# Kernel optimization log

Measured on AMD Instinct MI355X. Metric: run time of the kernel, lower is better.

## Reference

```python
import jax, jax.numpy as jnp
import numpy as np

B, N, D, H = 4, 2048, 512, 8
HEAD = D // H
TEMP = 8.0


def setup_inputs() -> dict:
    key = jax.random.key(0)
    k1, k2, k3, k4 = jax.random.split(key, 4)
    return {
        "keys": jax.random.normal(k1, (B, N, D), dtype=jnp.float32),
        "queries": jax.random.normal(k2, (B, N, D), dtype=jnp.float32),
        "values": jax.random.normal(k3, (B, N, D), dtype=jnp.float32),
        "W_comb": jax.random.normal(k4, (D, D), dtype=jnp.float32) * (1.0 / np.sqrt(D)),
        "b_comb": jnp.zeros((D,), dtype=jnp.float32),
    }


def reference(keys, queries, values, W_comb, b_comb):
    b, nk, d = keys.shape
    nq = queries.shape[1]
    h, hd = H, HEAD
    # split heads: (b, n, d) -> (b, n, h, hd)
    k = keys.reshape(b, nk, h, hd)
    q = queries.reshape(b, nq, h, hd)
    v = values.reshape(b, nk, h, hd)
    # scaled dot-product attention per head
    logits = jnp.einsum("bqhd,bkhd->bhqk", q, k) / TEMP  # (b, h, nq, nk)
    w = jax.nn.softmax(logits, axis=-1)
    out = jnp.einsum("bhqk,bkhd->bqhd", w, v).reshape(b, nq, d)
    # head_combine: Linear with bias (torch: x @ W.T + b)
    return out @ W_comb.T + b_comb
```

## Files before the change

### kernel.cpp

```cpp
#include <hip/hip_runtime.h>

#define B_ 4
#define N_ 2048
#define D_ 512
#define H_ 8

typedef __attribute__((ext_vector_type(8))) short bf16x8;
typedef __attribute__((ext_vector_type(4))) short bf16x4;
typedef __attribute__((ext_vector_type(4))) float f32x4;

__device__ __forceinline__ unsigned short f32_to_bf16(float f) {
  unsigned int u = __float_as_uint(f);
  u += 0x7FFFu + ((u >> 16) & 1u);
  return (unsigned short)(u >> 16);
}

__device__ __forceinline__ unsigned int pack2_bf16(float a, float b) {
#if __has_builtin(__builtin_amdgcn_cvt_pk_bf16_f32)
  typedef __attribute__((ext_vector_type(2))) __bf16 bf16v2;
  bf16v2 r = __builtin_amdgcn_cvt_pk_bf16_f32(a, b);
  return *(unsigned int*)&r;
#else
  return (unsigned int)f32_to_bf16(a) | ((unsigned int)f32_to_bf16(b) << 16);
#endif
}

__device__ __forceinline__ float fast_exp2(float x) {
#if __has_builtin(__builtin_amdgcn_exp2f)
  return __builtin_amdgcn_exp2f(x);
#else
  return exp2f(x);
#endif
}

__device__ __forceinline__ f32x4 mfma16(bf16x4 a, bf16x4 b, f32x4 c) {
#if __has_builtin(__builtin_amdgcn_mfma_f32_16x16x16_bf16)
  return __builtin_amdgcn_mfma_f32_16x16x16_bf16(a, b, c, 0, 0, 0);
#else
  return __builtin_amdgcn_mfma_f32_16x16x16bf16_1k(a, b, c, 0, 0, 0);
#endif
}

__global__ __launch_bounds__(256) void convert_kernel(
    const float* __restrict__ Kf, const float* __restrict__ Qf,
    const float* __restrict__ Vf, const float* __restrict__ Wf,
    unsigned short* __restrict__ Qb, unsigned short* __restrict__ Kb,
    unsigned short* __restrict__ Wb, unsigned short* __restrict__ Vt) {
  __shared__ float tile[64 * 72];
  const int tid = threadIdx.x;
  if (blockIdx.x < 1024) {
    const float qs = 0.125f * 1.4426950408889634f;
    int gid = blockIdx.x * 256 + tid;
    const float4* Q4 = (const float4*)Qf;
    const float4* K4 = (const float4*)Kf;
    for (int i = gid; i < (B_ * N_ * D_) / 4; i += 262144) {
      float4 q = Q4[i];
      ((uint2*)Qb)[i] = make_uint2(pack2_bf16(q.x * qs, q.y * qs),
                                   pack2_bf16(q.z * qs, q.w * qs));
      float4 k = K4[i];
      ((uint2*)Kb)[i] = make_uint2(pack2_bf16(k.x, k.y), pack2_bf16(k.z, k.w));
    }
    if (gid < (D_ * D_) / 4) {
      float4 w = ((const float4*)Wf)[gid];
      ((uint2*)Wb)[gid] = make_uint2(pack2_bf16(w.x, w.y), pack2_bf16(w.z, w.w));
    }
  } else {
    int bid = blockIdx.x - 1024;
    int nt = bid & 31, bh = bid >> 5;
    int b = bh >> 3, h = bh & 7;
    int n0 = nt * 64;
#pragma unroll
    for (int i = 0; i < 4; ++i) {
      int idx = i * 256 + tid;
      int r = idx >> 4, c = idx & 15;
      *(float4*)&tile[r * 72 + c * 4] =
          *(const float4*)(Vf + (size_t)(b * N_ + n0 + r) * D_ + h * 64 + c * 4);
    }
    __syncthreads();
    int d = tid >> 2, c = tid & 3;
    unsigned int o[8];
#pragma unroll
    for (int j = 0; j < 8; ++j)
      o[j] = pack2_bf16(tile[(c * 16 + 2 * j) * 72 + d],
                        tile[(c * 16 + 2 * j + 1) * 72 + d]);
    unsigned short* dst = Vt + ((size_t)bh * 64 + d) * N_ + n0 + c * 16;
    *(bf16x8*)dst = *(bf16x8*)&o[0];
    *(bf16x8*)(dst + 8) = *(bf16x8*)&o[4];
  }
}

__global__ __launch_bounds__(256, 2) void attn_kernel(
    const unsigned short* __restrict__ Qb, const unsigned short* __restrict__ Kb,
    const unsigned short* __restrict__ Vt, unsigned short* __restrict__ Ob) {
  __shared__ unsigned short Kl[2][64 * 72];
  __shared__ unsigned short Vl[2][64 * 72];

  const int tid = threadIdx.x;
  const int w = tid >> 6;
  const int lane = tid & 63;
  const int lr = lane & 15;
  const int lq = lane >> 4;

  const int bh = blockIdx.y;
  const int qb = blockIdx.x * 128;
  const size_t slab = (size_t)(bh >> 3) * N_ * D_ + (size_t)(bh & 7) * 64;
  const unsigned short* kbase = Kb + slab;
  const unsigned short* vtbase = Vt + (size_t)bh * 64 * N_;

  bf16x8 qa[2][2];
#pragma unroll
  for (int g = 0; g < 2; ++g) {
    const unsigned short* qrow =
        Qb + slab + (size_t)(qb + w * 32 + g * 16 + lr) * D_;
    qa[g][0] = *(const bf16x8*)(qrow + 8 * lq);
    qa[g][1] = *(const bf16x8*)(qrow + 32 + 8 * lq);
  }

  f32x4 O[4][2];
#pragma unroll
  for (int i = 0; i < 4; ++i)
#pragma unroll
    for (int g = 0; g < 2; ++g) O[i][g] = (f32x4){0.f, 0.f, 0.f, 0.f};
  float l_g[2] = {0.f, 0.f};

  const int st_r = tid >> 3;
  const int st_c = tid & 7;

  {
    const unsigned short* ksrc = kbase + (size_t)st_r * D_ + st_c * 8;
    bf16x8 a = *(const bf16x8*)ksrc;
    bf16x8 b = *(const bf16x8*)(ksrc + (size_t)32 * D_);
    const unsigned short* vsrc = vtbase + (size_t)st_r * N_ + st_c * 8;
    bf16x8 c = *(const bf16x8*)vsrc;
    bf16x8 d = *(const bf16x8*)(vsrc + (size_t)32 * N_);
    *(bf16x8*)&Kl[0][st_r * 72 + st_c * 8] = a;
    *(bf16x8*)&Kl[0][(st_r + 32) * 72 + st_c * 8] = b;
    *(bf16x8*)&Vl[0][st_r * 72 + st_c * 8] = c;
    *(bf16x8*)&Vl[0][(st_r + 32) * 72 + st_c * 8] = d;
  }

  for (int kt = 0; kt < 32; ++kt) {
    const int p = kt & 1;
    __syncthreads();

    bf16x8 nk0, nk1, nv0, nv1;
    const bool more = (kt + 1) < 32;
    if (more) {
      const int kb1 = (kt + 1) * 64;
      const unsigned short* ksrc = kbase + (size_t)(kb1 + st_r) * D_ + st_c * 8;
      nk0 = *(const bf16x8*)ksrc;
      nk1 = *(const bf16x8*)(ksrc + (size_t)32 * D_);
      const unsigned short* vsrc = vtbase + (size_t)st_r * N_ + kb1 + st_c * 8;
      nv0 = *(const bf16x8*)vsrc;
      nv1 = *(const bf16x8*)(vsrc + (size_t)32 * N_);
    }

    f32x4 S[4][2];
#pragma unroll
    for (int nt = 0; nt < 4; ++nt) {
      bf16x8 kf0 = *(const bf16x8*)&Kl[p][(nt * 16 + lr) * 72 + 8 * lq];
      bf16x8 kf1 = *(const bf16x8*)&Kl[p][(nt * 16 + lr) * 72 + 32 + 8 * lq];
#pragma unroll
      for (int g = 0; g < 2; ++g) {
        S[nt][g] = __builtin_amdgcn_mfma_f32_16x16x32_bf16(
            kf0, qa[g][0], (f32x4){0.f, 0.f, 0.f, 0.f}, 0, 0, 0);
        S[nt][g] = __builtin_amdgcn_mfma_f32_16x16x32_bf16(kf1, qa[g][1],
                                                           S[nt][g], 0, 0, 0);
      }
    }

    bf16x4 pf[4][2];
#pragma unroll
    for (int nt = 0; nt < 4; ++nt)
#pragma unroll
      for (int g = 0; g < 2; ++g) {
        float p0 = fast_exp2(S[nt][g][0]);
        float p1 = fast_exp2(S[nt][g][1]);
        float p2 = fast_exp2(S[nt][g][2]);
        float p3 = fast_exp2(S[nt][g][3]);
        l_g[g] += (p0 + p1) + (p2 + p3);
        uint2 packed = make_uint2(pack2_bf16(p0, p1), pack2_bf16(p2, p3));
        pf[nt][g] = *(bf16x4*)&packed;
      }

#pragma unroll
    for (int dt = 0; dt < 4; ++dt) {
#pragma unroll
      for (int nt = 0; nt < 4; ++nt) {
        bf16x4 vf =
            *(const bf16x4*)&Vl[p][(dt * 16 + lr) * 72 + nt * 16 + 4 * lq];
#pragma unroll
        for (int g = 0; g < 2; ++g)
          O[dt][g] = mfma16(vf, pf[nt][g], O[dt][g]);
      }
    }

    if (more) {
      *(bf16x8*)&Kl[1 - p][st_r * 72 + st_c * 8] = nk0;
      *(bf16x8*)&Kl[1 - p][(st_r + 32) * 72 + st_c * 8] = nk1;
      *(bf16x8*)&Vl[1 - p][st_r * 72 + st_c * 8] = nv0;
      *(bf16x8*)&Vl[1 - p][(st_r + 32) * 72 + st_c * 8] = nv1;
    }
  }

#pragma unroll
  for (int g = 0; g < 2; ++g) {
    l_g[g] += __shfl_xor(l_g[g], 16);
    l_g[g] += __shfl_xor(l_g[g], 32);
  }

  __syncthreads();
  unsigned short* SR = &Kl[0][0];
#pragma unroll
  for (int g = 0; g < 2; ++g) {
    float linv = 1.0f / l_g[g];
#pragma unroll
    for (int dt = 0; dt < 4; ++dt) {
      float v0 = O[dt][g][0] * linv;
      float v1 = O[dt][g][1] * linv;
      float v2 = O[dt][g][2] * linv;
      float v3 = O[dt][g][3] * linv;
      uint2 packed = make_uint2(pack2_bf16(v0, v1), pack2_bf16(v2, v3));
      *(bf16x4*)&SR[(w * 32 + g * 16 + lr) * 72 + dt * 16 + lq * 4] =
          *(bf16x4*)&packed;
    }
  }
  __syncthreads();
  {
    const int row = tid >> 1, half = tid & 1;
    unsigned short* dst = Ob + slab + (size_t)(qb + row) * D_ + half * 32;
    const unsigned short* src = &SR[row * 72 + half * 32];
    *(bf16x8*)dst = *(const bf16x8*)src;
    *(bf16x8*)(dst + 8) = *(const bf16x8*)(src + 8);
    *(bf16x8*)(dst + 16) = *(const bf16x8*)(src + 16);
    *(bf16x8*)(dst + 24) = *(const bf16x8*)(src + 24);
  }
}

__global__ __launch_bounds__(256) void gemm_kernel(
    const unsigned short* __restrict__ A, const unsigned short* __restrict__ Wb,
    const float* __restrict__ bias, float* __restrict__ out) {
  __shared__ unsigned short A_lds[2][64 * 72];
  __shared__ unsigned short W_lds[2][64 * 72];

  const int tid = threadIdx.x;
  const int w = tid >> 6;
  const int lane = tid & 63;
  const int lr = lane & 15;
  const int lq = lane >> 4;

  const int cb = blockIdx.x * 64;
  const int mb = blockIdx.y * 64;

  const int dc = (tid & 7) * 8;
  const int r0 = tid >> 3;

  f32x4 acc[4];
#pragma unroll
  for (int i = 0; i < 4; ++i) acc[i] = (f32x4){0.f, 0.f, 0.f, 0.f};

  {
    *(bf16x8*)&A_lds[0][r0 * 72 + dc] =
        *(const bf16x8*)(A + (size_t)(mb + r0) * D_ + dc);
    *(bf16x8*)&A_lds[0][(r0 + 32) * 72 + dc] =
        *(const bf16x8*)(A + (size_t)(mb + r0 + 32) * D_ + dc);
    *(bf16x8*)&W_lds[0][r0 * 72 + dc] =
        *(const bf16x8*)(Wb + (size_t)(cb + r0) * D_ + dc);
    *(bf16x8*)&W_lds[0][(r0 + 32) * 72 + dc] =
        *(const bf16x8*)(Wb + (size_t)(cb + r0 + 32) * D_ + dc);
  }

  for (int kt = 0; kt < 8; ++kt) {
    const int p = kt & 1;
    __syncthreads();

    bf16x8 na0, na1, nw0, nw1;
    const bool more = (kt + 1) < 8;
    if (more) {
      const int k1 = (kt + 1) * 64;
      na0 = *(const bf16x8*)(A + (size_t)(mb + r0) * D_ + k1 + dc);
      na1 = *(const bf16x8*)(A + (size_t)(mb + r0 + 32) * D_ + k1 + dc);
      nw0 = *(const bf16x8*)(Wb + (size_t)(cb + r0) * D_ + k1 + dc);
      nw1 = *(const bf16x8*)(Wb + (size_t)(cb + r0 + 32) * D_ + k1 + dc);
    }

    bf16x8 a0 = *(const bf16x8*)&A_lds[p][(w * 16 + lr) * 72 + 8 * lq];
    bf16x8 a1 = *(const bf16x8*)&A_lds[p][(w * 16 + lr) * 72 + 32 + 8 * lq];
#pragma unroll
    for (int nt = 0; nt < 4; ++nt) {
      bf16x8 b0 = *(const bf16x8*)&W_lds[p][(nt * 16 + lr) * 72 + 8 * lq];
      bf16x8 b1 = *(const bf16x8*)&W_lds[p][(nt * 16 + lr) * 72 + 32 + 8 * lq];
      acc[nt] = __builtin_amdgcn_mfma_f32_16x16x32_bf16(a0, b0, acc[nt], 0, 0, 0);
      acc[nt] = __builtin_amdgcn_mfma_f32_16x16x32_bf16(a1, b1, acc[nt], 0, 0, 0);
    }

    if (more) {
      *(bf16x8*)&A_lds[1 - p][r0 * 72 + dc] = na0;
      *(bf16x8*)&A_lds[1 - p][(r0 + 32) * 72 + dc] = na1;
      *(bf16x8*)&W_lds[1 - p][r0 * 72 + dc] = nw0;
      *(bf16x8*)&W_lds[1 - p][(r0 + 32) * 72 + dc] = nw1;
    }
  }

#pragma unroll
  for (int nt = 0; nt < 4; ++nt) {
    float bc = bias[cb + nt * 16 + lr];
#pragma unroll
    for (int rr = 0; rr < 4; ++rr) {
      int row = mb + w * 16 + lq * 4 + rr;
      out[(size_t)row * D_ + cb + nt * 16 + lr] = acc[nt][rr] + bc;
    }
  }
}

extern "C" void kernel_launch(void* const* d_in, const int* in_sizes, int n_in,
                              void* d_out, int out_size, void* d_ws,
                              size_t ws_size, hipStream_t stream) {
  (void)in_sizes; (void)n_in; (void)out_size; (void)ws_size;
  const float* keys    = (const float*)d_in[0];
  const float* queries = (const float*)d_in[1];
  const float* values  = (const float*)d_in[2];
  const float* W       = (const float*)d_in[3];
  const float* bias    = (const float*)d_in[4];
  float* out = (float*)d_out;

  char* ws = (char*)d_ws;
  unsigned short* Qb = (unsigned short*)(ws);
  unsigned short* Kb = (unsigned short*)(ws + 8388608);
  unsigned short* Vt = (unsigned short*)(ws + 16777216);
  unsigned short* Wb = (unsigned short*)(ws + 25165824);
  unsigned short* Ab = (unsigned short*)(ws + 25690112);

  convert_kernel<<<2048, 256, 0, stream>>>(keys, queries, values, W,
                                           Qb, Kb, Wb, Vt);

  attn_kernel<<<dim3(N_ / 128, B_ * H_), 256, 0, stream>>>(Qb, Kb, Vt, Ab);

  gemm_kernel<<<dim3(D_ / 64, (B_ * N_) / 64), 256, 0, stream>>>(Ab, Wb, bias,
                                                                 out);
}
```

Before: 166.0 us.

## Fuse Q/K/W fp32-to-bf16 conversion into attention and GEMM loaders

Removes the separate conversion pass for queries, keys and the combine weight; the attention kernel now loads fp32 Q and K directly and converts to bf16 while staging into registers and LDS, and the GEMM converts W on load. Only V still gets a standalone transpose-convert kernel. This drops a full write and re-read of bf16 Q/K copies. The cost is that K tiles are read as fp32 once per query block (16 times per head), which doubles global or L2 traffic for K in the attention loop and adds conversion ALU work inside it.

After: 186.2 us. 1.12x slower.

```diff
diff --git a/kernel.cpp b/kernel.cpp
--- a/kernel.cpp
+++ b/kernel.cpp
@@ -25,6 +25,15 @@
 #endif
 }
 
+__device__ __forceinline__ bf16x8 cvt8(float4 a, float4 b) {
+  unsigned int o[4];
+  o[0] = pack2_bf16(a.x, a.y);
+  o[1] = pack2_bf16(a.z, a.w);
+  o[2] = pack2_bf16(b.x, b.y);
+  o[3] = pack2_bf16(b.z, b.w);
+  return *(bf16x8*)&o[0];
+}
+
 __device__ __forceinline__ float fast_exp2(float x) {
 #if __has_builtin(__builtin_amdgcn_exp2f)
   return __builtin_amdgcn_exp2f(x);
@@ -41,56 +50,35 @@
 #endif
 }
 
-__global__ __launch_bounds__(256) void convert_kernel(
-    const float* __restrict__ Kf, const float* __restrict__ Qf,
-    const float* __restrict__ Vf, const float* __restrict__ Wf,
-    unsigned short* __restrict__ Qb, unsigned short* __restrict__ Kb,
-    unsigned short* __restrict__ Wb, unsigned short* __restrict__ Vt) {
+__global__ __launch_bounds__(256) void convert_v_kernel(
+    const float* __restrict__ Vf, unsigned short* __restrict__ Vt) {
   __shared__ float tile[64 * 72];
   const int tid = threadIdx.x;
-  if (blockIdx.x < 1024) {
-    const float qs = 0.125f * 1.4426950408889634f;
-    int gid = blockIdx.x * 256 + tid;
-    const float4* Q4 = (const float4*)Qf;
-    const float4* K4 = (const float4*)Kf;
-    for (int i = gid; i < (B_ * N_ * D_) / 4; i += 262144) {
-      float4 q = Q4[i];
-      ((uint2*)Qb)[i] = make_uint2(pack2_bf16(q.x * qs, q.y * qs),
-                                   pack2_bf16(q.z * qs, q.w * qs));
-      float4 k = K4[i];
-      ((uint2*)Kb)[i] = make_uint2(pack2_bf16(k.x, k.y), pack2_bf16(k.z, k.w));
-    }
-    if (gid < (D_ * D_) / 4) {
-      float4 w = ((const float4*)Wf)[gid];
-      ((uint2*)Wb)[gid] = make_uint2(pack2_bf16(w.x, w.y), pack2_bf16(w.z, w.w));
-    }
-  } else {
-    int bid = blockIdx.x - 1024;
-    int nt = bid & 31, bh = bid >> 5;
-    int b = bh >> 3, h = bh & 7;
-    int n0 = nt * 64;
-#pragma unroll
-    for (int i = 0; i < 4; ++i) {
-      int idx = i * 256 + tid;
-      int r = idx >> 4, c = idx & 15;
-      *(float4*)&tile[r * 72 + c * 4] =
-          *(const float4*)(Vf + (size_t)(b * N_ + n0 + r) * D_ + h * 64 + c * 4);
-    }
-    __syncthreads();
-    int d = tid >> 2, c = tid & 3;
-    unsigned int o[8];
-#pragma unroll
-    for (int j = 0; j < 8; ++j)
-      o[j] = pack2_bf16(tile[(c * 16 + 2 * j) * 72 + d],
-                        tile[(c * 16 + 2 * j + 1) * 72 + d]);
-    unsigned short* dst = Vt + ((size_t)bh * 64 + d) * N_ + n0 + c * 16;
-    *(bf16x8*)dst = *(bf16x8*)&o[0];
-    *(bf16x8*)(dst + 8) = *(bf16x8*)&o[4];
-  }
+  int bid = blockIdx.x;
+  int nt = bid & 31, bh = bid >> 5;
+  int b = bh >> 3, h = bh & 7;
+  int n0 = nt * 64;
+#pragma unroll
+  for (int i = 0; i < 4; ++i) {
+    int idx = i * 256 + tid;
+    int r = idx >> 4, c = idx & 15;
+    *(float4*)&tile[r * 72 + c * 4] =
+        *(const float4*)(Vf + (size_t)(b * N_ + n0 + r) * D_ + h * 64 + c * 4);
+  }
+  __syncthreads();
+  int d = tid >> 2, c = tid & 3;
+  unsigned int o[8];
+#pragma unroll
+  for (int j = 0; j < 8; ++j)
+    o[j] = pack2_bf16(tile[(c * 16 + 2 * j) * 72 + d],
+                      tile[(c * 16 + 2 * j + 1) * 72 + d]);
+  unsigned short* dst = Vt + ((size_t)bh * 64 + d) * N_ + n0 + c * 16;
+  *(bf16x8*)dst = *(bf16x8*)&o[0];
+  *(bf16x8*)(dst + 8) = *(bf16x8*)&o[4];
 }
 
 __global__ __launch_bounds__(256, 2) void attn_kernel(
-    const unsigned short* __restrict__ Qb, const unsigned short* __restrict__ Kb,
+    const float* __restrict__ Qf, const float* __restrict__ Kf,
     const unsigned short* __restrict__ Vt, unsigned short* __restrict__ Ob) {
   __shared__ unsigned short Kl[2][64 * 72];
   __shared__ unsigned short Vl[2][64 * 72];
@@ -104,16 +92,22 @@
   const int bh = blockIdx.y;
   const int qb = blockIdx.x * 128;
   const size_t slab = (size_t)(bh >> 3) * N_ * D_ + (size_t)(bh & 7) * 64;
-  const unsigned short* kbase = Kb + slab;
+  const float* kbase = Kf + slab;
   const unsigned short* vtbase = Vt + (size_t)bh * 64 * N_;
 
+  const float qs = 0.125f * 1.4426950408889634f;
   bf16x8 qa[2][2];
 #pragma unroll
   for (int g = 0; g < 2; ++g) {
-    const unsigned short* qrow =
-        Qb + slab + (size_t)(qb + w * 32 + g * 16 + lr) * D_;
-    qa[g][0] = *(const bf16x8*)(qrow + 8 * lq);
-    qa[g][1] = *(const bf16x8*)(qrow + 32 + 8 * lq);
+    const float* qrow = Qf + slab + (size_t)(qb + w * 32 + g * 16 + lr) * D_;
+#pragma unroll
+    for (int hf = 0; hf < 2; ++hf) {
+      float4 x = *(const float4*)(qrow + hf * 32 + 8 * lq);
+      float4 y = *(const float4*)(qrow + hf * 32 + 8 * lq + 4);
+      x.x *= qs; x.y *= qs; x.z *= qs; x.w *= qs;
+      y.x *= qs; y.y *= qs; y.z *= qs; y.w *= qs;
+      qa[g][hf] = cvt8(x, y);
+    }
   }
 
   f32x4 O[4][2];
@@ -127,14 +121,16 @@
   const int st_c = tid & 7;
 
   {
-    const unsigned short* ksrc = kbase + (size_t)st_r * D_ + st_c * 8;
-    bf16x8 a = *(const bf16x8*)ksrc;
-    bf16x8 b = *(const bf16x8*)(ksrc + (size_t)32 * D_);
+    const float* ksrc = kbase + (size_t)st_r * D_ + st_c * 8;
+    float4 a0 = *(const float4*)ksrc;
+    float4 a1 = *(const float4*)(ksrc + 4);
+    float4 b0 = *(const float4*)(ksrc + (size_t)32 * D_);
+    float4 b1 = *(const float4*)(ksrc + (size_t)32 * D_ + 4);
     const unsigned short* vsrc = vtbase + (size_t)st_r * N_ + st_c * 8;
     bf16x8 c = *(const bf16x8*)vsrc;
     bf16x8 d = *(const bf16x8*)(vsrc + (size_t)32 * N_);
-    *(bf16x8*)&Kl[0][st_r * 72 + st_c * 8] = a;
-    *(bf16x8*)&Kl[0][(st_r + 32) * 72 + st_c * 8] = b;
+    *(bf16x8*)&Kl[0][st_r * 72 + st_c * 8] = cvt8(a0, a1);
+    *(bf16x8*)&Kl[0][(st_r + 32) * 72 + st_c * 8] = cvt8(b0, b1);
     *(bf16x8*)&Vl[0][st_r * 72 + st_c * 8] = c;
     *(bf16x8*)&Vl[0][(st_r + 32) * 72 + st_c * 8] = d;
   }
@@ -143,14 +139,17 @@
     const int p = kt & 1;
     __syncthreads();
 
-    bf16x8 nk0, nk1, nv0, nv1;
+    float4 ka0, ka1, kb0, kb1;
+    bf16x8 nv0, nv1;
     const bool more = (kt + 1) < 32;
     if (more) {
-      const int kb1 = (kt + 1) * 64;
-      const unsigned short* ksrc = kbase + (size_t)(kb1 + st_r) * D_ + st_c * 8;
-      nk0 = *(const bf16x8*)ksrc;
-      nk1 = *(const bf16x8*)(ksrc + (size_t)32 * D_);
-      const unsigned short* vsrc = vtbase + (size_t)st_r * N_ + kb1 + st_c * 8;
+      const int kb1i = (kt + 1) * 64;
+      const float* ksrc = kbase + (size_t)(kb1i + st_r) * D_ + st_c * 8;
+      ka0 = *(const float4*)ksrc;
+      ka1 = *(const float4*)(ksrc + 4);
+      kb0 = *(const float4*)(ksrc + (size_t)32 * D_);
+      kb1 = *(const float4*)(ksrc + (size_t)32 * D_ + 4);
+      const unsigned short* vsrc = vtbase + (size_t)st_r * N_ + kb1i + st_c * 8;
       nv0 = *(const bf16x8*)vsrc;
       nv1 = *(const bf16x8*)(vsrc + (size_t)32 * N_);
     }
@@ -196,8 +195,8 @@
     }
 
     if (more) {
-      *(bf16x8*)&Kl[1 - p][st_r * 72 + st_c * 8] = nk0;
-      *(bf16x8*)&Kl[1 - p][(st_r + 32) * 72 + st_c * 8] = nk1;
+      *(bf16x8*)&Kl[1 - p][st_r * 72 + st_c * 8] = cvt8(ka0, ka1);
+      *(bf16x8*)&Kl[1 - p][(st_r + 32) * 72 + st_c * 8] = cvt8(kb0, kb1);
       *(bf16x8*)&Vl[1 - p][st_r * 72 + st_c * 8] = nv0;
       *(bf16x8*)&Vl[1 - p][(st_r + 32) * 72 + st_c * 8] = nv1;
     }
@@ -238,7 +237,7 @@
 }
 
 __global__ __launch_bounds__(256) void gemm_kernel(
-    const unsigned short* __restrict__ A, const unsigned short* __restrict__ Wb,
+    const unsigned short* __restrict__ A, const float* __restrict__ Wf,
     const float* __restrict__ bias, float* __restrict__ out) {
   __shared__ unsigned short A_lds[2][64 * 72];
   __shared__ unsigned short W_lds[2][64 * 72];
@@ -264,24 +263,31 @@
         *(const bf16x8*)(A + (size_t)(mb + r0) * D_ + dc);
     *(bf16x8*)&A_lds[0][(r0 + 32) * 72 + dc] =
         *(const bf16x8*)(A + (size_t)(mb + r0 + 32) * D_ + dc);
-    *(bf16x8*)&W_lds[0][r0 * 72 + dc] =
-        *(const bf16x8*)(Wb + (size_t)(cb + r0) * D_ + dc);
-    *(bf16x8*)&W_lds[0][(r0 + 32) * 72 + dc] =
-        *(const bf16x8*)(Wb + (size_t)(cb + r0 + 32) * D_ + dc);
+    const float* wsrc = Wf + (size_t)(cb + r0) * D_ + dc;
+    float4 w0a = *(const float4*)wsrc;
+    float4 w0b = *(const float4*)(wsrc + 4);
+    float4 w1a = *(const float4*)(wsrc + (size_t)32 * D_);
+    float4 w1b = *(const float4*)(wsrc + (size_t)32 * D_ + 4);
+    *(bf16x8*)&W_lds[0][r0 * 72 + dc] = cvt8(w0a, w0b);
+    *(bf16x8*)&W_lds[0][(r0 + 32) * 72 + dc] = cvt8(w1a, w1b);
   }
 
   for (int kt = 0; kt < 8; ++kt) {
     const int p = kt & 1;
     __syncthreads();
 
-    bf16x8 na0, na1, nw0, nw1;
+    bf16x8 na0, na1;
+    float4 w0a, w0b, w1a, w1b;
     const bool more = (kt + 1) < 8;
     if (more) {
       const int k1 = (kt + 1) * 64;
       na0 = *(const bf16x8*)(A + (size_t)(mb + r0) * D_ + k1 + dc);
       na1 = *(const bf16x8*)(A + (size_t)(mb + r0 + 32) * D_ + k1 + dc);
-      nw0 = *(const bf16x8*)(Wb + (size_t)(cb + r0) * D_ + k1 + dc);
-      nw1 = *(const bf16x8*)(Wb + (size_t)(cb + r0 + 32) * D_ + k1 + dc);
+      const float* wsrc = Wf + (size_t)(cb + r0) * D_ + k1 + dc;
+      w0a = *(const float4*)wsrc;
+      w0b = *(const float4*)(wsrc + 4);
+      w1a = *(const float4*)(wsrc + (size_t)32 * D_);
+      w1b = *(const float4*)(wsrc + (size_t)32 * D_ + 4);
     }
 
     bf16x8 a0 = *(const bf16x8*)&A_lds[p][(w * 16 + lr) * 72 + 8 * lq];
@@ -297,8 +303,8 @@
     if (more) {
       *(bf16x8*)&A_lds[1 - p][r0 * 72 + dc] = na0;
       *(bf16x8*)&A_lds[1 - p][(r0 + 32) * 72 + dc] = na1;
-      *(bf16x8*)&W_lds[1 - p][r0 * 72 + dc] = nw0;
-      *(bf16x8*)&W_lds[1 - p][(r0 + 32) * 72 + dc] = nw1;
+      *(bf16x8*)&W_lds[1 - p][r0 * 72 + dc] = cvt8(w0a, w0b);
+      *(bf16x8*)&W_lds[1 - p][(r0 + 32) * 72 + dc] = cvt8(w1a, w1b);
     }
   }
 
@@ -325,17 +331,14 @@
   float* out = (float*)d_out;
 
   char* ws = (char*)d_ws;
-  unsigned short* Qb = (unsigned short*)(ws);
-  unsigned short* Kb = (unsigned short*)(ws + 8388608);
-  unsigned short* Vt = (unsigned short*)(ws + 16777216);
-  unsigned short* Wb = (unsigned short*)(ws + 25165824);
-  unsigned short* Ab = (unsigned short*)(ws + 25690112);
-
-  convert_kernel<<<2048, 256, 0, stream>>>(keys, queries, values, W,
-                                           Qb, Kb, Wb, Vt);
-
-  attn_kernel<<<dim3(N_ / 128, B_ * H_), 256, 0, stream>>>(Qb, Kb, Vt, Ab);
-
-  gemm_kernel<<<dim3(D_ / 64, (B_ * N_) / 64), 256, 0, stream>>>(Ab, Wb, bias,
+  unsigned short* Vt = (unsigned short*)(ws);
+  unsigned short* Ab = (unsigned short*)(ws + 8388608);
+
+  convert_v_kernel<<<1024, 256, 0, stream>>>(values, Vt);
+
+  attn_kernel<<<dim3(N_ / 128, B_ * H_), 256, 0, stream>>>(queries, keys, Vt,
+                                                           Ab);
+
+  gemm_kernel<<<dim3(D_ / 64, (B_ * N_) / 64), 256, 0, stream>>>(Ab, W, bias,
                                                                  out);
 }
```
